# Performance work log

Hardware: AMD Instinct MI355X
Metric: run time of the kernel (lower is better)

## Reference

```python
import jax, jax.numpy as jnp
import numpy as np

NX = 32; NY = 32; D = 2; K = 5; SCALE = 1.0
DX = 2.0 * SCALE / (NX - 1)
N = NX * NY

def _region_kernel():
    # kernel_size^d grid of offsets with spacing DX, centered at 0
    t = (jnp.arange(K, dtype=jnp.float32) - (K - 1) / 2.0) * DX
    gx, gy = jnp.meshgrid(t, t, indexing='ij')
    return jnp.stack((gx, gy), -1).reshape(-1, D)  # (K*K, 2)

def _build_cov(scaling, transform):
    # lower-triangular L: diag = scaling, strict lower = transform; cov = L L^T
    L = jnp.zeros((scaling.shape[0], D, D), scaling.dtype)
    L = L.at[:, 0, 0].set(scaling[:, 0])
    L = L.at[:, 1, 1].set(scaling[:, 1])
    L = L.at[:, 1, 0].set(transform[:, 0])
    return L @ jnp.swapaxes(L, -1, -2)

def reference(means, u, scaling, transform, conv_w, conv_b, emb_w, emb_b,
              lin1_w, lin1_b, sol_w, sol_b, tr_w, tr_b, sc_w, sc_b, tf_w, tf_b):
    cov = _build_cov(scaling, transform)          # (N,2,2)
    conics = jnp.linalg.inv(cov)                  # (N,2,2)
    # local sample gather: every Gaussian contributes K*K sample points
    samples = (means[:, None, :] + _region_kernel()[None]).reshape(-1, D)  # (S,2)
    # global Gaussian mixture evaluation at all sample points (no_grad in torch)
    diff = samples[:, None, :] - means[None, :, :]            # (S,N,2)
    Cd = jnp.einsum('nde,sne->snd', conics, diff)             # (S,N,2)
    G = jnp.exp(-0.5 * jnp.einsum('snd,snd->sn', diff, Cd))   # (S,N) densities
    w = G * u[None, :, 0]                                     # (S,N)
    u_s = jnp.sum(w, -1, keepdims=True)                       # (S,1)
    # Hessian of mixture: sum_j w_j ((C_j d)(C_j d)^T - C_j)
    wc = w[..., None] * Cd
    uxx = jnp.einsum('snd,sne->sde', wc, Cd) - jnp.einsum('sn,nde->sde', w, conics)
    pde = (uxx[:, 0, 0] + uxx[:, 1, 1])[:, None]              # diffusion rhs = laplacian
    mask = jnp.all(jnp.abs(samples) < SCALE, -1)[:, None].astype(u.dtype)
    img = jnp.concatenate((u_s, pde, mask), -1)               # (S, 3)
    img = img.reshape(N, K * K, 3).transpose(0, 2, 1).reshape(N, 3, K, K)
    img = jax.lax.stop_gradient(img)  # torch computes samples under no_grad
    params = jnp.concatenate((means, u, scaling, transform), -1)  # (N,6)
    # 4 stacked Networks (solution, translation, scale, transform); conv kernel
    # spans the whole K x K patch so Conv2d reduces to a tensordot
    y = jnp.tanh(jnp.einsum('ichw,mochw->mio', img, conv_w) + conv_b[:, None, :])
    e = jnp.tanh(jnp.einsum('ip,mpq->miq', params, emb_w) + emb_b[:, None, :])
    h = jnp.concatenate((y, e), -1)                               # (4,N,80)
    h = jnp.tanh(jnp.einsum('mio,moq->miq', h, lin1_w) + lin1_b[:, None, :])
    u_new = u + (h[0] @ sol_w + sol_b)
    means_new = means + (h[1] @ tr_w + tr_b)
    scaling_new = scaling * jnp.exp(h[2] @ sc_w + sc_b)
    transform_new = transform + (h[3] @ tf_w + tf_b)
    return jnp.concatenate((u_new, means_new, scaling_new, transform_new), -1)  # (N,6)

def setup_inputs() -> dict:
    key = jax.random.key(0)
    ks = jax.random.split(key, 14)
    tx = jnp.linspace(-1.0, 1.0, NX, dtype=jnp.float32) * SCALE
    ty = jnp.linspace(-1.0, 1.0, NY, dtype=jnp.float32) * SCALE
    gx, gy = jnp.meshgrid(tx, ty, indexing='ij')
    means = jnp.stack((gx, gy), -1).reshape(-1, D)
    scaling = jnp.full((N, D), float(np.exp(-4.5)) * SCALE, dtype=jnp.float32)
    transform = jnp.zeros((N, 1), jnp.float32)
    # initial u: gaussian bump (as in the torch __init__ default branch)
    u = jnp.exp(-0.5 * (means ** 2).sum(-1) / (0.1 * SCALE))[:, None].astype(jnp.float32)
    def p(k, shape, s):
        return jax.random.normal(k, shape, jnp.float32) * s
    return {
        'means': means, 'u': u, 'scaling': scaling, 'transform': transform,
        'conv_w': p(ks[0], (4, 50, 3, K, K), 0.08), 'conv_b': p(ks[1], (4, 50), 0.02),
        'emb_w': p(ks[2], (4, 6, 30), 0.3), 'emb_b': p(ks[3], (4, 30), 0.02),
        'lin1_w': p(ks[4], (4, 80, 80), 0.1), 'lin1_b': p(ks[5], (4, 80), 0.02),
        'sol_w': p(ks[6], (80, 1), 0.1), 'sol_b': jnp.zeros((1,), jnp.float32),
        'tr_w': p(ks[7], (80, 2), 0.1), 'tr_b': jnp.zeros((2,), jnp.float32),
        'sc_w': p(ks[8], (80, 2), 0.1), 'sc_b': jnp.zeros((2,), jnp.float32),
        'tf_w': p(ks[9], (80, 1), 0.1), 'tf_b': jnp.zeros((1,), jnp.float32),
    }
```

## Files before the change

### kernel.cpp

```cpp
#include <hip/hip_runtime.h>
#include <math.h>


namespace {

constexpr int NG = 1024;
constexpr float DXF = 2.0f / 31.0f;
constexpr float NHALF_LOG2E = -0.72134752044448170367f;
constexpr float TWO_LOG2E   = 2.88539008177792681472f;
constexpr float LOG2E       = 1.44269504088896340736f;
constexpr float QCUT        = 80.0f;

__device__ __forceinline__ float fast_tanh(float x) {
  x = fminf(9.0f, fmaxf(-9.0f, x));
  float t = __builtin_amdgcn_exp2f(TWO_LOG2E * x);
  return (t - 1.0f) * __builtin_amdgcn_rcpf(t + 1.0f);
}

__global__ __launch_bounds__(256) void k_prep(
    const float* __restrict__ conv_w, float* __restrict__ cwT)
{
  int idx = blockIdx.x * 256 + threadIdx.x;
  if (idx < 4 * 75 * 50) {
    int m = idx / 3750, r = idx - m * 3750;
    int c = r / 50, o = r - c * 50;
    cwT[idx] = conv_w[(m * 50 + o) * 75 + c];
  }
}

__global__ __launch_bounds__(256) void k_fused(
    const float* __restrict__ means, const float* __restrict__ uu,
    const float* __restrict__ scaling, const float* __restrict__ transform,
    const float* __restrict__ cwT, const float* __restrict__ conv_b,
    const float* __restrict__ emb_w, const float* __restrict__ emb_b,
    const float* __restrict__ lin1_w, const float* __restrict__ lin1_b,
    const float* __restrict__ sol_w, const float* __restrict__ sol_b,
    const float* __restrict__ tr_w, const float* __restrict__ tr_b,
    const float* __restrict__ sc_w, const float* __restrict__ sc_b,
    const float* __restrict__ tf_w, const float* __restrict__ tf_b,
    float* __restrict__ out)
{
  __shared__ float4 sgp[NG];
  __shared__ float2 sgq[NG];
  __shared__ int s_cnt;
  __shared__ float r_us[10][25];
  __shared__ float r_pde[10][25];
  __shared__ float simg[75];
  __shared__ float sparams[6];
  __shared__ float h[320];
  __shared__ float h2[320];
  __shared__ float hpart[6][8];

  const int i = blockIdx.x;
  const int tid = threadIdx.x;

  if (tid == 0) s_cnt = 0;
  if (tid < 6) {
    float v;
    if (tid < 2)       v = means[2 * i + tid];
    else if (tid == 2) v = uu[i];
    else if (tid < 5)  v = scaling[2 * i + (tid - 3)];
    else               v = transform[i];
    sparams[tid] = v;
  }
  __syncthreads();

  const float mxi = sparams[0], myi = sparams[1];
  for (int g = tid; g < NG; g += 256) {
    float gmx = means[2 * g], gmy = means[2 * g + 1];
    float s0 = scaling[2 * g], s1 = scaling[2 * g + 1];
    float t0 = transform[g];
    float ex = fmaxf(fabsf(gmx - mxi) - 2.0f * DXF, 0.0f);
    float ey = fmaxf(fabsf(gmy - myi) - 2.0f * DXF, 0.0f);
    float tr = s0 * s0 + s1 * s1 + t0 * t0;
    if (ex * ex + ey * ey <= QCUT * tr) {
      int idx = atomicAdd(&s_cnt, 1);
      float cc  = 1.0f / (s1 * s1);
      float is0 = 1.0f / s0;
      float bb  = -t0 * cc * is0;
      float aa  = (t0 * t0 * cc + 1.0f) * is0 * is0;
      sgp[idx] = make_float4(gmx, gmy, aa, bb);
      sgq[idx] = make_float2(cc, uu[g]);
    }
  }
  __syncthreads();

  const int cnt = s_cnt;
  if (tid < 250) {
    const int c = tid / 25;
    const int s = tid - c * 25;
    const int kx = s / 5, ky = s - kx * 5;
    const float sx = mxi + (float)(kx - 2) * DXF;
    const float sy = myi + (float)(ky - 2) * DXF;
    float us = 0.0f, pde = 0.0f;
    for (int j = c; j < cnt; j += 10) {
      float4 p  = sgp[j];
      float2 qv = sgq[j];
      float dx = sx - p.x, dy = sy - p.y;
      float a = p.z, b = p.w, cc = qv.x;
      float Cd0 = a * dx + b * dy;
      float Cd1 = b * dx + cc * dy;
      float q   = dx * Cd0 + dy * Cd1;
      float w   = qv.y * __builtin_amdgcn_exp2f(NHALF_LOG2E * q);
      us  += w;
      pde += w * (Cd0 * Cd0 + Cd1 * Cd1 - (a + cc));
    }
    r_us[c][s]  = us;
    r_pde[c][s] = pde;
  }
  __syncthreads();

  if (tid < 25) {
    float U = 0.0f, P = 0.0f;
#pragma unroll
    for (int c = 0; c < 10; ++c) { U += r_us[c][tid]; P += r_pde[c][tid]; }
    const int kx = tid / 5, ky = tid - kx * 5;
    const float sx = mxi + (float)(kx - 2) * DXF;
    const float sy = myi + (float)(ky - 2) * DXF;
    simg[tid]      = U;
    simg[25 + tid] = P;
    simg[50 + tid] = (fabsf(sx) < 1.0f && fabsf(sy) < 1.0f) ? 1.0f : 0.0f;
  }
  __syncthreads();

  if (tid < 200) {
    const int m = tid / 50, o = tid - m * 50;
    const float* w = cwT + m * 3750 + o;
    float acc = conv_b[m * 50 + o];
#pragma unroll
    for (int c = 0; c < 75; ++c) acc = fmaf(simg[c], w[c * 50], acc);
    h[m * 80 + o] = fast_tanh(acc);
  }
  if (tid >= 200) {
    for (int e = tid - 200; e < 120; e += 56) {
      const int m = e / 30, q = e - m * 30;
      float acc = emb_b[m * 30 + q];
#pragma unroll
      for (int p = 0; p < 6; ++p) acc = fmaf(sparams[p], emb_w[(m * 6 + p) * 30 + q], acc);
      h[m * 80 + 50 + q] = fast_tanh(acc);
    }
  }
  __syncthreads();

  for (int idx = tid; idx < 320; idx += 256) {
    const int m = idx / 80, q = idx - m * 80;
    const float* lw = lin1_w + m * 6400 + q;
    const float* hh = h + m * 80;
    float acc = lin1_b[m * 80 + q];
#pragma unroll 8
    for (int j = 0; j < 80; ++j) acc = fmaf(hh[j], lw[j * 80], acc);
    h2[idx] = fast_tanh(acc);
  }
  __syncthreads();

  if (tid < 48) {
    const int o = tid >> 3, c8 = tid & 7;
    const int m = (o == 0) ? 0 : (o < 3) ? 1 : (o < 5) ? 2 : 3;
    const float* wp; int stride;
    if (o == 0)      { wp = sol_w;            stride = 1; }
    else if (o < 3)  { wp = tr_w + (o - 1);   stride = 2; }
    else if (o < 5)  { wp = sc_w + (o - 3);   stride = 2; }
    else             { wp = tf_w;             stride = 1; }
    const float* hh = h2 + m * 80;
    float acc = 0.0f;
    const int j0 = c8 * 10;
#pragma unroll
    for (int j = 0; j < 10; ++j) acc = fmaf(hh[j0 + j], wp[(j0 + j) * stride], acc);
    hpart[o][c8] = acc;
  }
  __syncthreads();

  if (tid < 6) {
    float acc = 0.0f;
#pragma unroll
    for (int c = 0; c < 8; ++c) acc += hpart[tid][c];
    float res;
    if (tid == 0)      res = sparams[2] + acc + sol_b[0];
    else if (tid < 3)  res = sparams[tid - 1] + acc + tr_b[tid - 1];
    else if (tid < 5)  res = sparams[tid] * __builtin_amdgcn_exp2f(LOG2E * (acc + sc_b[tid - 3]));
    else               res = sparams[5] + acc + tf_b[0];
    out[i * 6 + tid] = res;
  }
}

}

extern "C" void kernel_launch(void* const* d_in, const int* in_sizes, int n_in,
                              void* d_out, int out_size, void* d_ws, size_t ws_size,
                              hipStream_t stream) {
  const float* means     = (const float*)d_in[0];
  const float* uu        = (const float*)d_in[1];
  const float* scaling   = (const float*)d_in[2];
  const float* transform = (const float*)d_in[3];
  const float* conv_w    = (const float*)d_in[4];
  const float* conv_b    = (const float*)d_in[5];
  const float* emb_w     = (const float*)d_in[6];
  const float* emb_b     = (const float*)d_in[7];
  const float* lin1_w    = (const float*)d_in[8];
  const float* lin1_b    = (const float*)d_in[9];
  const float* sol_w     = (const float*)d_in[10];
  const float* sol_b     = (const float*)d_in[11];
  const float* tr_w      = (const float*)d_in[12];
  const float* tr_b      = (const float*)d_in[13];
  const float* sc_w      = (const float*)d_in[14];
  const float* sc_b      = (const float*)d_in[15];
  const float* tf_w      = (const float*)d_in[16];
  const float* tf_b      = (const float*)d_in[17];

  float* cwT = (float*)d_ws;
  float* out = (float*)d_out;

  k_prep<<<59, 256, 0, stream>>>(conv_w, cwT);
  k_fused<<<1024, 256, 0, stream>>>(means, uu, scaling, transform,
                                    cwT, conv_b, emb_w, emb_b, lin1_w, lin1_b,
                                    sol_w, sol_b, tr_w, tr_b, sc_w, sc_b, tf_w, tf_b,
                                    out);
}
```

Measured before the change: 101.8 us.

## Process four Gaussians per block and share weights across them

Each block now handles four Gaussians with 512 threads. The union bounding box is used for one shared neighbour cull. Conv weights are staged into shared memory once per block, replacing the separate transpose kernel. Every MLP weight load is reused across the four accumulators. The intent is to amortise the global weight traffic, the culling pass and a kernel launch over more work. In exchange there are only 256 blocks, a looser cull that yields more candidates per sample, and a large shared-memory footprint (about 30KB of conv weights) that may limit occupancy.

```diff
diff --git a/kernel.cpp b/kernel.cpp
--- a/kernel.cpp
+++ b/kernel.cpp
@@ -5,6 +5,7 @@
 namespace {
 
 constexpr int NG = 1024;
+constexpr int G  = 4;
 constexpr float DXF = 2.0f / 31.0f;
 constexpr float NHALF_LOG2E = -0.72134752044448170367f;
 constexpr float TWO_LOG2E   = 2.88539008177792681472f;
@@ -17,21 +18,10 @@
   return (t - 1.0f) * __builtin_amdgcn_rcpf(t + 1.0f);
 }
 
-__global__ __launch_bounds__(256) void k_prep(
-    const float* __restrict__ conv_w, float* __restrict__ cwT)
-{
-  int idx = blockIdx.x * 256 + threadIdx.x;
-  if (idx < 4 * 75 * 50) {
-    int m = idx / 3750, r = idx - m * 3750;
-    int c = r / 50, o = r - c * 50;
-    cwT[idx] = conv_w[(m * 50 + o) * 75 + c];
-  }
-}
-
-__global__ __launch_bounds__(256) void k_fused(
+__global__ __launch_bounds__(512) void k_fused(
     const float* __restrict__ means, const float* __restrict__ uu,
     const float* __restrict__ scaling, const float* __restrict__ transform,
-    const float* __restrict__ cwT, const float* __restrict__ conv_b,
+    const float* __restrict__ conv_w, const float* __restrict__ conv_b,
     const float* __restrict__ emb_w, const float* __restrict__ emb_b,
     const float* __restrict__ lin1_w, const float* __restrict__ lin1_b,
     const float* __restrict__ sol_w, const float* __restrict__ sol_b,
@@ -40,60 +30,78 @@
     const float* __restrict__ tf_w, const float* __restrict__ tf_b,
     float* __restrict__ out)
 {
+  __shared__ float  scw[4 * 50 * 75];
   __shared__ float4 sgp[NG];
   __shared__ float2 sgq[NG];
   __shared__ int s_cnt;
-  __shared__ float r_us[10][25];
-  __shared__ float r_pde[10][25];
-  __shared__ float simg[75];
-  __shared__ float sparams[6];
-  __shared__ float h[320];
-  __shared__ float h2[320];
-  __shared__ float hpart[6][8];
-
-  const int i = blockIdx.x;
+  __shared__ float r_us[5][100];
+  __shared__ float r_pde[5][100];
+  __shared__ float simg[G][75];
+  __shared__ float sparams[G][6];
+  __shared__ float h[G][320];
+  __shared__ float h2[G][320];
+  __shared__ float hpart[G][6][8];
+
+  const int i0 = blockIdx.x * G;
   const int tid = threadIdx.x;
 
+  {
+    const float4* src = (const float4*)conv_w;
+    float4* dst = (float4*)scw;
+    for (int idx = tid; idx < 3750; idx += 512) dst[idx] = src[idx];
+  }
   if (tid == 0) s_cnt = 0;
-  if (tid < 6) {
+  if (tid < G * 6) {
+    const int g = tid / 6, f = tid - g * 6, ig = i0 + g;
     float v;
-    if (tid < 2)       v = means[2 * i + tid];
-    else if (tid == 2) v = uu[i];
-    else if (tid < 5)  v = scaling[2 * i + (tid - 3)];
-    else               v = transform[i];
-    sparams[tid] = v;
-  }
-  __syncthreads();
-
-  const float mxi = sparams[0], myi = sparams[1];
-  for (int g = tid; g < NG; g += 256) {
-    float gmx = means[2 * g], gmy = means[2 * g + 1];
-    float s0 = scaling[2 * g], s1 = scaling[2 * g + 1];
+    if (f < 2)       v = means[2 * ig + f];
+    else if (f == 2) v = uu[ig];
+    else if (f < 5)  v = scaling[2 * ig + (f - 3)];
+    else             v = transform[ig];
+    sparams[g][f] = v;
+  }
+  __syncthreads();
+
+  float lox = 1e30f, hix = -1e30f, loy = 1e30f, hiy = -1e30f;
+#pragma unroll
+  for (int g = 0; g < G; ++g) {
+    lox = fminf(lox, sparams[g][0]); hix = fmaxf(hix, sparams[g][0]);
+    loy = fminf(loy, sparams[g][1]); hiy = fmaxf(hiy, sparams[g][1]);
+  }
+  lox -= 2.0f * DXF; hix += 2.0f * DXF;
+  loy -= 2.0f * DXF; hiy += 2.0f * DXF;
+
+  const float2* means2 = (const float2*)means;
+  const float2* scal2  = (const float2*)scaling;
+  for (int g = tid; g < NG; g += 512) {
+    float2 mg = means2[g];
+    float2 sg = scal2[g];
     float t0 = transform[g];
-    float ex = fmaxf(fabsf(gmx - mxi) - 2.0f * DXF, 0.0f);
-    float ey = fmaxf(fabsf(gmy - myi) - 2.0f * DXF, 0.0f);
-    float tr = s0 * s0 + s1 * s1 + t0 * t0;
+    float ex = fmaxf(fmaxf(lox - mg.x, mg.x - hix), 0.0f);
+    float ey = fmaxf(fmaxf(loy - mg.y, mg.y - hiy), 0.0f);
+    float tr = sg.x * sg.x + sg.y * sg.y + t0 * t0;
     if (ex * ex + ey * ey <= QCUT * tr) {
       int idx = atomicAdd(&s_cnt, 1);
-      float cc  = 1.0f / (s1 * s1);
-      float is0 = 1.0f / s0;
+      float cc  = 1.0f / (sg.y * sg.y);
+      float is0 = 1.0f / sg.x;
       float bb  = -t0 * cc * is0;
       float aa  = (t0 * t0 * cc + 1.0f) * is0 * is0;
-      sgp[idx] = make_float4(gmx, gmy, aa, bb);
+      sgp[idx] = make_float4(mg.x, mg.y, aa, bb);
       sgq[idx] = make_float2(cc, uu[g]);
     }
   }
   __syncthreads();
 
   const int cnt = s_cnt;
-  if (tid < 250) {
-    const int c = tid / 25;
-    const int s = tid - c * 25;
-    const int kx = s / 5, ky = s - kx * 5;
-    const float sx = mxi + (float)(kx - 2) * DXF;
-    const float sy = myi + (float)(ky - 2) * DXF;
+  if (tid < 500) {
+    const int c = tid / 100;
+    const int s = tid - c * 100;
+    const int g = s / 25, k = s - g * 25;
+    const int kx = k / 5, ky = k - kx * 5;
+    const float sx = sparams[g][0] + (float)(kx - 2) * DXF;
+    const float sy = sparams[g][1] + (float)(ky - 2) * DXF;
     float us = 0.0f, pde = 0.0f;
-    for (int j = c; j < cnt; j += 10) {
+    for (int j = c; j < cnt; j += 5) {
       float4 p  = sgp[j];
       float2 qv = sgq[j];
       float dx = sx - p.x, dy = sy - p.y;
@@ -110,76 +118,95 @@
   }
   __syncthreads();
 
-  if (tid < 25) {
+  if (tid < 100) {
+    const int g = tid / 25, k = tid - g * 25;
     float U = 0.0f, P = 0.0f;
 #pragma unroll
-    for (int c = 0; c < 10; ++c) { U += r_us[c][tid]; P += r_pde[c][tid]; }
-    const int kx = tid / 5, ky = tid - kx * 5;
-    const float sx = mxi + (float)(kx - 2) * DXF;
-    const float sy = myi + (float)(ky - 2) * DXF;
-    simg[tid]      = U;
-    simg[25 + tid] = P;
-    simg[50 + tid] = (fabsf(sx) < 1.0f && fabsf(sy) < 1.0f) ? 1.0f : 0.0f;
+    for (int c = 0; c < 5; ++c) { U += r_us[c][tid]; P += r_pde[c][tid]; }
+    const int kx = k / 5, ky = k - kx * 5;
+    const float sx = sparams[g][0] + (float)(kx - 2) * DXF;
+    const float sy = sparams[g][1] + (float)(ky - 2) * DXF;
+    simg[g][k]      = U;
+    simg[g][25 + k] = P;
+    simg[g][50 + k] = (fabsf(sx) < 1.0f && fabsf(sy) < 1.0f) ? 1.0f : 0.0f;
   }
   __syncthreads();
 
   if (tid < 200) {
     const int m = tid / 50, o = tid - m * 50;
-    const float* w = cwT + m * 3750 + o;
-    float acc = conv_b[m * 50 + o];
-#pragma unroll
-    for (int c = 0; c < 75; ++c) acc = fmaf(simg[c], w[c * 50], acc);
-    h[m * 80 + o] = fast_tanh(acc);
-  }
-  if (tid >= 200) {
-    for (int e = tid - 200; e < 120; e += 56) {
-      const int m = e / 30, q = e - m * 30;
-      float acc = emb_b[m * 30 + q];
-#pragma unroll
-      for (int p = 0; p < 6; ++p) acc = fmaf(sparams[p], emb_w[(m * 6 + p) * 30 + q], acc);
-      h[m * 80 + 50 + q] = fast_tanh(acc);
-    }
-  }
-  __syncthreads();
-
-  for (int idx = tid; idx < 320; idx += 256) {
-    const int m = idx / 80, q = idx - m * 80;
+    const float* w = scw + (m * 50 + o) * 75;
+    const float bb = conv_b[m * 50 + o];
+    float acc[G] = {bb, bb, bb, bb};
+#pragma unroll 5
+    for (int c = 0; c < 75; ++c) {
+      float wv = w[c];
+#pragma unroll
+      for (int g = 0; g < G; ++g) acc[g] = fmaf(simg[g][c], wv, acc[g]);
+    }
+#pragma unroll
+    for (int g = 0; g < G; ++g) h[g][m * 80 + o] = fast_tanh(acc[g]);
+  }
+  if (tid >= 200 && tid < 320) {
+    const int e = tid - 200;
+    const int m = e / 30, q = e - m * 30;
+    const float bb = emb_b[m * 30 + q];
+    float acc[G] = {bb, bb, bb, bb};
+#pragma unroll
+    for (int p = 0; p < 6; ++p) {
+      float wv = emb_w[(m * 6 + p) * 30 + q];
+#pragma unroll
+      for (int g = 0; g < G; ++g) acc[g] = fmaf(sparams[g][p], wv, acc[g]);
+    }
+#pragma unroll
+    for (int g = 0; g < G; ++g) h[g][m * 80 + 50 + q] = fast_tanh(acc[g]);
+  }
+  __syncthreads();
+
+  if (tid < 320) {
+    const int m = tid / 80, q = tid - m * 80;
     const float* lw = lin1_w + m * 6400 + q;
-    const float* hh = h + m * 80;
-    float acc = lin1_b[m * 80 + q];
+    const float bb = lin1_b[m * 80 + q];
+    float acc[G] = {bb, bb, bb, bb};
 #pragma unroll 8
-    for (int j = 0; j < 80; ++j) acc = fmaf(hh[j], lw[j * 80], acc);
-    h2[idx] = fast_tanh(acc);
-  }
-  __syncthreads();
-
-  if (tid < 48) {
-    const int o = tid >> 3, c8 = tid & 7;
+    for (int j = 0; j < 80; ++j) {
+      float wv = lw[j * 80];
+#pragma unroll
+      for (int g = 0; g < G; ++g) acc[g] = fmaf(h[g][m * 80 + j], wv, acc[g]);
+    }
+#pragma unroll
+    for (int g = 0; g < G; ++g) h2[g][m * 80 + q] = fast_tanh(acc[g]);
+  }
+  __syncthreads();
+
+  if (tid < 192) {
+    const int g = tid / 48, t = tid - g * 48;
+    const int o = t >> 3, c8 = t & 7;
     const int m = (o == 0) ? 0 : (o < 3) ? 1 : (o < 5) ? 2 : 3;
     const float* wp; int stride;
     if (o == 0)      { wp = sol_w;            stride = 1; }
     else if (o < 3)  { wp = tr_w + (o - 1);   stride = 2; }
     else if (o < 5)  { wp = sc_w + (o - 3);   stride = 2; }
     else             { wp = tf_w;             stride = 1; }
-    const float* hh = h2 + m * 80;
+    const float* hh = h2[g] + m * 80;
     float acc = 0.0f;
     const int j0 = c8 * 10;
 #pragma unroll
     for (int j = 0; j < 10; ++j) acc = fmaf(hh[j0 + j], wp[(j0 + j) * stride], acc);
-    hpart[o][c8] = acc;
-  }
-  __syncthreads();
-
-  if (tid < 6) {
+    hpart[g][o][c8] = acc;
+  }
+  __syncthreads();
+
+  if (tid < G * 6) {
+    const int g = tid / 6, o = tid - g * 6;
     float acc = 0.0f;
 #pragma unroll
-    for (int c = 0; c < 8; ++c) acc += hpart[tid][c];
+    for (int c = 0; c < 8; ++c) acc += hpart[g][o][c];
     float res;
-    if (tid == 0)      res = sparams[2] + acc + sol_b[0];
-    else if (tid < 3)  res = sparams[tid - 1] + acc + tr_b[tid - 1];
-    else if (tid < 5)  res = sparams[tid] * __builtin_amdgcn_exp2f(LOG2E * (acc + sc_b[tid - 3]));
-    else               res = sparams[5] + acc + tf_b[0];
-    out[i * 6 + tid] = res;
+    if (o == 0)      res = sparams[g][2] + acc + sol_b[0];
+    else if (o < 3)  res = sparams[g][o - 1] + acc + tr_b[o - 1];
+    else if (o < 5)  res = sparams[g][o] * __builtin_amdgcn_exp2f(LOG2E * (acc + sc_b[o - 3]));
+    else             res = sparams[g][5] + acc + tf_b[0];
+    out[(i0 + g) * 6 + o] = res;
   }
 }
 
@@ -207,12 +234,10 @@
   const float* tf_w      = (const float*)d_in[16];
   const float* tf_b      = (const float*)d_in[17];
 
-  float* cwT = (float*)d_ws;
   float* out = (float*)d_out;
 
-  k_prep<<<59, 256, 0, stream>>>(conv_w, cwT);
-  k_fused<<<1024, 256, 0, stream>>>(means, uu, scaling, transform,
-                                    cwT, conv_b, emb_w, emb_b, lin1_w, lin1_b,
-                                    sol_w, sol_b, tr_w, tr_b, sc_w, sc_b, tf_w, tf_b,
-                                    out);
-}
+  k_fused<<<NG / G, 512, 0, stream>>>(means, uu, scaling, transform,
+                                      conv_w, conv_b, emb_w, emb_b, lin1_w, lin1_b,
+                                      sol_w, sol_b, tr_w, tr_b, sc_w, sc_b, tf_w, tf_b,
+                                      out);
+}
```

Result: faster. 98.23 us (-3.5%).
